# Optimization experiments

Hardware: AMD Instinct MI355X
Metric: run time of the kernel (lower is better)

Reference implementation:

```python
import jax, jax.numpy as jnp
import numpy as np

N = 100000          # nodes
E = 1_600_000       # edges (avg degree 16)
IN, H, OUT = 64, 128, 64


def _gcn(x, src, tgt, w, W, b, n):
    """PyG GCNConv with add_self_loops=True and edge weights.
    Zero-weight edges contribute nothing to degree or aggregation, so the
    torch code's boolean edge masking is reproduced exactly by zeroed weights.
    """
    h = x @ W.T                                           # [n, out]
    deg = jax.ops.segment_sum(w, tgt, num_segments=n) + 1.0  # +1 self-loop weight
    dinv = jnp.where(deg > 0, jax.lax.rsqrt(deg), 0.0)    # [n]
    norm = dinv[src] * w * dinv[tgt]                      # [e]
    agg = jax.ops.segment_sum(h[src] * norm[:, None], tgt, num_segments=n)
    # self-loop message: h_i * dinv_i * 1 * dinv_i
    return agg + h * (dinv * dinv)[:, None] + b


def setup_inputs() -> dict:
    key = jax.random.key(0)
    ks = jax.random.split(key, 12)
    def lin(k, o, i):
        return jax.random.normal(k, (o, i), dtype=jnp.float32) / np.sqrt(i)
    return {
        "x": jax.random.normal(ks[0], (N, IN), dtype=jnp.float32),
        "edge_index": jax.random.randint(ks[1], (2, E), 0, N),
        "edge_weight": jax.random.normal(ks[2], (E,), dtype=jnp.float32),
        "W1p": lin(ks[3], H, IN),  "b1p": jnp.zeros((H,), jnp.float32),
        "W1n": lin(ks[4], H, IN),  "b1n": jnp.zeros((H,), jnp.float32),
        "W2p": lin(ks[5], OUT, H), "b2p": jnp.zeros((OUT,), jnp.float32),
        "W2n": lin(ks[6], OUT, H), "b2n": jnp.zeros((OUT,), jnp.float32),
    }


def reference(x, edge_index, edge_weight, W1p, b1p, W1n, b1n, W2p, b2p, W2n, b2n):
    src, tgt = edge_index[0], edge_index[1]
    n = x.shape[0]
    wp = jnp.where(edge_weight >= 0, edge_weight, 0.0)    # pos subgraph
    wn = jnp.where(edge_weight < 0, -edge_weight, 0.0)    # |neg| subgraph
    h = jax.nn.relu(_gcn(x, src, tgt, wp, W1p, b1p, n)
                    - _gcn(x, src, tgt, wn, W1n, b1n, n))
    out = jax.nn.relu(_gcn(h, src, tgt, wp, W2p, b2p, n)
                      - _gcn(h, src, tgt, wn, W2n, b2n, n))
    return out
```

## Files before the change

kernel.cpp:

```cpp
#include <hip/hip_runtime.h>
#include <hip/hip_fp16.h>
#include <cstddef>

#define TPB 256
#define BSH 9
#define BTGT 512
#define EPA 16
#define ACHUNK (EPA * TPB)
#define LSTR 160
#define CAP 10240

typedef _Float16 f16x8 __attribute__((ext_vector_type(8)));
typedef float    f32x4 __attribute__((ext_vector_type(4)));

__global__ __launch_bounds__(256) void bucket_scatter_kernel(
        const int* __restrict__ tgt, const int* __restrict__ src,
        const float* __restrict__ ew, int* __restrict__ cnt_pad,
        int2* __restrict__ recs, int E) {
    __shared__ int lcnt[256];
    __shared__ int lbase[256];
    const int tid = threadIdx.x;
    lcnt[tid] = 0;
    __syncthreads();
    const int base = blockIdx.x * ACHUNK + tid;
    int px[EPA], pw[EPA], mr[EPA], mb[EPA];
#pragma unroll
    for (int j = 0; j < EPA; ++j) {
        int e = base + j * TPB;
        if (e < E) {
            int t = tgt[e], s = src[e];
            float w = ew[e];
            int flag = (w < 0.0f) ? 1 : 0;
            mb[j] = t >> BSH;
            px[j] = ((t & (BTGT - 1)) << 23) | (s << 6) | flag;
            pw[j] = __float_as_int(w);
            mr[j] = atomicAdd(&lcnt[mb[j]], 1);
        }
    }
    __syncthreads();
    if (lcnt[tid]) lbase[tid] = atomicAdd(&cnt_pad[tid * 16], lcnt[tid]);
    __syncthreads();
#pragma unroll
    for (int j = 0; j < EPA; ++j) {
        int e = base + j * TPB;
        if (e < E) {
            int sl = lbase[mb[j]] + mr[j];
            if (sl < CAP)
                recs[(size_t)mb[j] * CAP + sl] = make_int2(px[j], pw[j]);
        }
    }
}

__global__ __launch_bounds__(512) void csr_build_kernel(
        const int* __restrict__ cnt_pad, const int2* __restrict__ recs,
        int2* __restrict__ rowse, int2* __restrict__ edat,
        float* __restrict__ dinvp, float* __restrict__ dinvn,
        const float* __restrict__ x,
        const float* __restrict__ W1p, const float* __restrict__ W1n,
        const float* __restrict__ W2p, const float* __restrict__ W2n,
        __half* __restrict__ xs, __half* __restrict__ w16, int n) {
    __shared__ int   hcnt[BTGT];
    __shared__ int   cur[BTGT];
    __shared__ int   sm[BTGT];
    __shared__ float sdp[BTGT];
    __shared__ float sdn[BTGT];
    const int b = blockIdx.x, tid = threadIdx.x;
    int cnt = cnt_pad[b * 16]; if (cnt > CAP) cnt = CAP;
    const int beg = b * CAP, end = beg + cnt;
    hcnt[tid] = 0;
    sdp[tid] = 0.f;
    sdn[tid] = 0.f;
    __syncthreads();
    for (int i = beg + tid; i < end; i += 512) {
        int2 r = recs[i];
        int tl = ((unsigned)r.x) >> 23;
        atomicAdd(&hcnt[tl], 1);
        float w = __int_as_float(r.y);
        if (w > 0.0f)      atomicAdd(&sdp[tl], w);
        else if (w < 0.0f) atomicAdd(&sdn[tl], -w);
    }
    __syncthreads();
    int own = hcnt[tid];
    sm[tid] = own;
    __syncthreads();
#pragma unroll
    for (int off = 1; off < 512; off <<= 1) {
        int add = (tid >= off) ? sm[tid - off] : 0;
        __syncthreads();
        sm[tid] += add;
        __syncthreads();
    }
    int excl = sm[tid] - own;
    cur[tid] = beg + excl;
    const int t0 = b << BSH;
    const int t = t0 + tid;
    if (t < n) {
        rowse[t] = make_int2(beg + excl, beg + excl + own);
        float dp = rsqrtf(sdp[tid] + 1.0f);
        float dn = rsqrtf(sdn[tid] + 1.0f);
        dinvp[t] = dp; dinvn[t] = dn;
        sdp[tid] = dp; sdn[tid] = dn;
    }
    __syncthreads();
    for (int i = beg + tid; i < end; i += 512) {
        int2 r = recs[i];
        int tl = ((unsigned)r.x) >> 23;
        int slot = atomicAdd(&cur[tl], 1);
        float w = __int_as_float(r.y);
        int flag = r.x & 1;
        float nv = w * (flag ? sdn[tl] : sdp[tl]);
        int srcflag = (((r.x >> 6) & 0x1FFFF) << 8) | (flag << 7) | flag;
        edat[slot] = make_int2(srcflag, __float_as_int(nv));
    }
    for (int it = tid; it < (BTGT << 5); it += 512) {
        int j = it >> 5, jp = it & 31;
        int tt = t0 + j;
        if (tt >= n) continue;
        float2 v = *(const float2*)(x + (size_t)tt * 64 + jp * 2);
        float dp = sdp[j], dn = sdn[j];
        __half2* xr = (__half2*)(xs + (size_t)tt * 128);
        xr[jp]      = __floats2half2_rn(v.x * dp, v.y * dp);
        xr[jp + 32] = __floats2half2_rn(v.x * dn, v.y * dn);
    }
    if (b == 0) {
        for (int q = tid; q < 16384; q += 512) {
            const float* Wsrc = (q < 4096) ? W1p : (q < 8192) ? W1n
                              : (q < 12288) ? W2p : W2n;
            float2 v = *(const float2*)(Wsrc + (size_t)(q & 4095) * 2);
            ((__half2*)w16)[q] = __floats2half2_rn(v.x, v.y);
        }
    }
}

__global__ __launch_bounds__(256) void gatherX_kernel(
        const int2* __restrict__ rowse, const int2* __restrict__ edat,
        const __half* __restrict__ xs,
        const float* __restrict__ dinvp, const float* __restrict__ dinvn,
        __half* __restrict__ agg, int n) {
    const int lane = threadIdx.x & 63;
    int t = (blockIdx.x * blockDim.x + threadIdx.x) >> 6;
    if (t >= n) return;
    t = __builtin_amdgcn_readfirstlane(t);
    const char* xB = (const char*)xs;
    int2 se = rowse[t];
    int beg = se.x, end = se.y;
    float aP[8], aN[8];
#pragma unroll
    for (int j = 0; j < 8; ++j) { aP[j] = 0.f; aN[j] = 0.f; }
    int e = beg;
    for (; e + 7 < end; e += 8) {
        unsigned long long dv[8];
#pragma unroll
        for (int j = 0; j < 8; ++j)
            dv[j] = __builtin_nontemporal_load(
                        (const unsigned long long*)(edat + e + j));
        const __half* r[8];
        float nvv[8];
        int fl[8];
#pragma unroll
        for (int j = 0; j < 8; ++j) {
            unsigned dx = (unsigned)dv[j];
            r[j]   = (const __half*)(xB + (dx & 0xFFFFFF80u));
            nvv[j] = __int_as_float((int)(dv[j] >> 32));
            fl[j]  = dx & 1;
        }
#pragma unroll
        for (int j = 0; j < 8; ++j) {
            float c = __half2float(r[j][lane]) * nvv[j];
            if (fl[j]) aN[j] += c; else aP[j] += c;
        }
    }
    for (; e + 3 < end; e += 4) {
        unsigned long long dv[4];
#pragma unroll
        for (int j = 0; j < 4; ++j)
            dv[j] = __builtin_nontemporal_load(
                        (const unsigned long long*)(edat + e + j));
#pragma unroll
        for (int j = 0; j < 4; ++j) {
            unsigned dx = (unsigned)dv[j];
            const __half* r = (const __half*)(xB + (dx & 0xFFFFFF80u));
            float c = __half2float(r[lane]) * __int_as_float((int)(dv[j] >> 32));
            if (dx & 1) aN[j] += c; else aP[j] += c;
        }
    }
    for (; e < end; ++e) {
        unsigned long long dv = __builtin_nontemporal_load(
                                    (const unsigned long long*)(edat + e));
        unsigned dx = (unsigned)dv;
        const __half* r = (const __half*)(xB + (dx & 0xFFFFFF80u));
        float c = __half2float(r[lane]) * __int_as_float((int)(dv >> 32));
        if (dx & 1) aN[0] += c; else aP[0] += c;
    }
    float accP = ((aP[0] + aP[1]) + (aP[2] + aP[3]))
               + ((aP[4] + aP[5]) + (aP[6] + aP[7]));
    float accN = ((aN[0] + aN[1]) + (aN[2] + aN[3]))
               + ((aN[4] + aN[5]) + (aN[6] + aN[7]));
    float sp = dinvp[t], sn = dinvn[t];
    accP += sp * __half2float(xs[(size_t)t * 128 + lane]);
    accN -= sn * __half2float(xs[(size_t)t * 128 + 64 + lane]);
    __builtin_nontemporal_store(__half_as_ushort((__half)accP),
        (unsigned short*)(agg + (size_t)t * 128 + lane));
    __builtin_nontemporal_store(__half_as_ushort((__half)accN),
        (unsigned short*)(agg + (size_t)t * 128 + 64 + lane));
}

__global__ __launch_bounds__(256) void gemm12_mfma(
        const __half* agg,
        const __half* __restrict__ w1p, const __half* __restrict__ w1n,
        const float* __restrict__ b1p, const float* __restrict__ b1n,
        const __half* __restrict__ w2p, const __half* __restrict__ w2n,
        const float* __restrict__ dinvp, const float* __restrict__ dinvn,
        __half* g2, int n) {
    __shared__ _Float16 tile[4][16 * LSTR];
    const int lane = threadIdx.x & 63;
    const int wv = threadIdx.x >> 6;
    _Float16* T = tile[wv];
    const int m = lane & 15, quad = lane >> 4;
    const int row0 = (blockIdx.x * 4 + wv) * 16;
    if (row0 >= n) return;
    int arow = row0 + m; if (arow > n - 1) arow = n - 1;

    f32x4 acc[8];
#pragma unroll
    for (int t = 0; t < 8; ++t) acc[t] = (f32x4){0.f, 0.f, 0.f, 0.f};
#pragma unroll
    for (int kc = 0; kc < 4; ++kc) {
        f16x8 a = *(const f16x8*)(agg + (size_t)arow * 128 + kc * 32 + quad * 8);
        const __half* W = (kc < 2) ? w1p : w1n;
        const int ko = (kc & 1) * 32 + quad * 8;
#pragma unroll
        for (int t = 0; t < 8; ++t) {
            f16x8 bfr = *(const f16x8*)(W + (size_t)(t * 16 + m) * 64 + ko);
            acc[t] = __builtin_amdgcn_mfma_f32_16x16x32_f16(a, bfr, acc[t], 0, 0, 0);
        }
    }
#pragma unroll
    for (int t = 0; t < 8; ++t) {
        int col = t * 16 + m;
        float bd = b1p[col] - b1n[col];
#pragma unroll
        for (int r = 0; r < 4; ++r)
            T[(quad * 4 + r) * LSTR + col] = (_Float16)fmaxf(acc[t][r] + bd, 0.f);
    }

    f32x4 acc2[8];
#pragma unroll
    for (int t = 0; t < 8; ++t) acc2[t] = (f32x4){0.f, 0.f, 0.f, 0.f};
#pragma unroll
    for (int kc = 0; kc < 4; ++kc) {
        f16x8 a = *(const f16x8*)(T + m * LSTR + kc * 32 + quad * 8);
#pragma unroll
        for (int t = 0; t < 8; ++t) {
            const __half* W = (t < 4) ? w2p : w2n;
            f16x8 bfr = *(const f16x8*)(W + (size_t)((t & 3) * 16 + m) * 128 + kc * 32 + quad * 8);
            acc2[t] = __builtin_amdgcn_mfma_f32_16x16x32_f16(a, bfr, acc2[t], 0, 0, 0);
        }
    }
    float sp[4], sn[4]; int rows[4];
#pragma unroll
    for (int r = 0; r < 4; ++r) {
        int rw = row0 + quad * 4 + r;
        rows[r] = rw;
        sp[r] = (rw < n) ? dinvp[rw] : 0.f;
        sn[r] = (rw < n) ? dinvn[rw] : 0.f;
    }
#pragma unroll
    for (int t = 0; t < 8; ++t) {
        int col = (t < 4 ? 0 : 64) + (t & 3) * 16 + m;
#pragma unroll
        for (int r = 0; r < 4; ++r)
            if (rows[r] < n) {
                float s = (t < 4) ? sp[r] : sn[r];
                g2[(size_t)rows[r] * 128 + col] = (__half)(acc2[t][r] * s);
            }
    }
}

__global__ __launch_bounds__(256) void gather64_kernel(
        const int2* __restrict__ rowse, const int2* __restrict__ edat,
        const __half* __restrict__ g2,
        const float* __restrict__ dinvp, const float* __restrict__ dinvn,
        const float* __restrict__ bp, const float* __restrict__ bn,
        float* __restrict__ out, int n) {
    const int lane = threadIdx.x & 63;
    int t = (blockIdx.x * blockDim.x + threadIdx.x) >> 6;
    if (t >= n) return;
    t = __builtin_amdgcn_readfirstlane(t);
    const char* gB = (const char*)g2;
    int2 se = rowse[t];
    int beg = se.x, end = se.y;
    float ac[8];
#pragma unroll
    for (int j = 0; j < 8; ++j) ac[j] = 0.f;
    int e = beg;
    for (; e + 7 < end; e += 8) {
        unsigned long long dv[8];
#pragma unroll
        for (int j = 0; j < 8; ++j)
            dv[j] = __builtin_nontemporal_load(
                        (const unsigned long long*)(edat + e + j));
#pragma unroll
        for (int j = 0; j < 8; ++j) {
            unsigned dx = (unsigned)dv[j];
            const __half* r = (const __half*)(gB + (dx & 0xFFFFFF80u));
            ac[j] += __half2float(r[lane]) * __int_as_float((int)(dv[j] >> 32));
        }
    }
    for (; e + 3 < end; e += 4) {
        unsigned long long dv[4];
#pragma unroll
        for (int j = 0; j < 4; ++j)
            dv[j] = __builtin_nontemporal_load(
                        (const unsigned long long*)(edat + e + j));
#pragma unroll
        for (int j = 0; j < 4; ++j) {
            unsigned dx = (unsigned)dv[j];
            const __half* r = (const __half*)(gB + (dx & 0xFFFFFF80u));
            ac[j] += __half2float(r[lane]) * __int_as_float((int)(dv[j] >> 32));
        }
    }
    for (; e < end; ++e) {
        unsigned long long dv = __builtin_nontemporal_load(
                                    (const unsigned long long*)(edat + e));
        unsigned dx = (unsigned)dv;
        const __half* r = (const __half*)(gB + (dx & 0xFFFFFF80u));
        ac[0] += __half2float(r[lane]) * __int_as_float((int)(dv >> 32));
    }
    float acc = ((ac[0] + ac[1]) + (ac[2] + ac[3]))
              + ((ac[4] + ac[5]) + (ac[6] + ac[7]));
    const float dp = dinvp[t], dn = dinvn[t];
    float hpv = __half2float(g2[(size_t)t * 128 + lane]);
    float hnv = __half2float(g2[(size_t)t * 128 + 64 + lane]);
    float o = acc + hpv * dp + bp[lane] - hnv * dn - bn[lane];
    __builtin_nontemporal_store(fmaxf(o, 0.f), out + (size_t)t * 64 + lane);
}

extern "C" void kernel_launch(void* const* d_in, const int* in_sizes, int n_in,
                              void* d_out, int out_size, void* d_ws, size_t ws_size,
                              hipStream_t stream) {
    const float* x   = (const float*)d_in[0];
    const int*   ei  = (const int*)d_in[1];
    const float* ew  = (const float*)d_in[2];
    const float* W1p = (const float*)d_in[3];
    const float* b1p = (const float*)d_in[4];
    const float* W1n = (const float*)d_in[5];
    const float* b1n = (const float*)d_in[6];
    const float* W2p = (const float*)d_in[7];
    const float* b2p = (const float*)d_in[8];
    const float* W2n = (const float*)d_in[9];
    const float* b2n = (const float*)d_in[10];

    const int E = in_sizes[2];
    const int n = in_sizes[0] / 64;
    const int nb = (n + BTGT - 1) >> BSH;
    const int* src = ei;
    const int* tgt = ei + E;

    int* wsi     = (int*)d_ws;
    int* cnt_pad = wsi;
    size_t o = 4096;
    int2*  rowse  = (int2*)(wsi + o);   o += 2 * (size_t)n;
    float* dinvp  = (float*)(wsi + o);  o += n;
    float* dinvn  = (float*)(wsi + o);  o += n;
    o = (o + 3) & ~(size_t)3;
    __half* xs  = (__half*)(wsi + o);   o += (size_t)n * 64;
    __half* w16 = (__half*)(wsi + o);   o += 16384;
    __half* w1p16 = w16, *w1n16 = w16 + 8192, *w2p16 = w16 + 16384, *w2n16 = w16 + 24576;
    int2* recs = (int2*)(wsi + o);      o += 2 * (size_t)nb * CAP;
    int2* edat = (int2*)(wsi + o);      o += 2 * (size_t)nb * CAP;
    __half* agg = (__half*)(wsi + o);   o += (size_t)n * 64;
    __half* g2  = agg;
    float*  out = (float*)d_out;

    hipMemsetAsync(cnt_pad, 0, 4096 * sizeof(int), stream);

    const int gridA = (E + ACHUNK - 1) / ACHUNK;
    const int gridW = (n * 64 + TPB - 1) / TPB;
    const int gridF = (n + 63) / 64;

    bucket_scatter_kernel<<<gridA, TPB, 0, stream>>>(tgt, src, ew, cnt_pad, recs, E);
    csr_build_kernel<<<nb, 512, 0, stream>>>(cnt_pad, recs, rowse, edat,
                                             dinvp, dinvn, x,
                                             W1p, W1n, W2p, W2n, xs, w16, n);
    gatherX_kernel<<<gridW, TPB, 0, stream>>>(rowse, edat, xs, dinvp, dinvn, agg, n);
    gemm12_mfma<<<gridF, TPB, 0, stream>>>(agg, w1p16, w1n16, b1p, b1n,
                                           w2p16, w2n16, dinvp, dinvn, g2, n);
    gather64_kernel<<<gridW, TPB, 0, stream>>>(rowse, edat, g2, dinvp, dinvn,
                                               b2p, b2n, out, n);
}
```

Before: 328.0 us.

## Make fused GEMM kernel persistent with register-resident weights and next-tile prefetch

Rewrites the two-layer MFMA GEMM so that each block handles one 16-row tile at a time, with its four waves splitting the output columns. Each wave loads its weight fragments into registers once, and the block loops over tiles with a grid-stride loop capped at a fixed grid size. The next tile's input rows are prefetched while the current tile is stored to shared memory, and the shared tile is shrunk and shared by the block. This is meant to cut repeated weight loads and overlap input loads with compute. In exchange it adds two block-wide barriers per tile and lowers parallelism per tile.

New measurement: 298.2 us. -9.1%, faster.

```diff
diff --git a/kernel.cpp b/kernel.cpp
--- a/kernel.cpp
+++ b/kernel.cpp
@@ -7,8 +7,9 @@
 #define BTGT 512
 #define EPA 16
 #define ACHUNK (EPA * TPB)
-#define LSTR 160
+#define LSTR 136
 #define CAP 10240
+#define GGRID 1024
 
 typedef _Float16 f16x8 __attribute__((ext_vector_type(8)));
 typedef float    f32x4 __attribute__((ext_vector_type(4)));
@@ -205,75 +206,95 @@
         (unsigned short*)(agg + (size_t)t * 128 + 64 + lane));
 }
 
-__global__ __launch_bounds__(256) void gemm12_mfma(
+__global__ __launch_bounds__(256, 2) void gemm12_mfma(
         const __half* agg,
         const __half* __restrict__ w1p, const __half* __restrict__ w1n,
         const float* __restrict__ b1p, const float* __restrict__ b1n,
         const __half* __restrict__ w2p, const __half* __restrict__ w2n,
         const float* __restrict__ dinvp, const float* __restrict__ dinvn,
         __half* g2, int n) {
-    __shared__ _Float16 tile[4][16 * LSTR];
+    __shared__ _Float16 T[16 * LSTR];
     const int lane = threadIdx.x & 63;
     const int wv = threadIdx.x >> 6;
-    _Float16* T = tile[wv];
     const int m = lane & 15, quad = lane >> 4;
-    const int row0 = (blockIdx.x * 4 + wv) * 16;
-    if (row0 >= n) return;
-    int arow = row0 + m; if (arow > n - 1) arow = n - 1;
-
-    f32x4 acc[8];
-#pragma unroll
-    for (int t = 0; t < 8; ++t) acc[t] = (f32x4){0.f, 0.f, 0.f, 0.f};
+    const int t0 = 2 * wv, t1 = t0 + 1;
+    const int ntile = (n + 15) >> 4;
+
+    f16x8 B1a[4], B1b[4], B2a[4], B2b[4];
+    const __half* W2 = (t0 < 4) ? w2p : w2n;
 #pragma unroll
     for (int kc = 0; kc < 4; ++kc) {
-        f16x8 a = *(const f16x8*)(agg + (size_t)arow * 128 + kc * 32 + quad * 8);
-        const __half* W = (kc < 2) ? w1p : w1n;
+        const __half* W1 = (kc < 2) ? w1p : w1n;
         const int ko = (kc & 1) * 32 + quad * 8;
-#pragma unroll
-        for (int t = 0; t < 8; ++t) {
-            f16x8 bfr = *(const f16x8*)(W + (size_t)(t * 16 + m) * 64 + ko);
-            acc[t] = __builtin_amdgcn_mfma_f32_16x16x32_f16(a, bfr, acc[t], 0, 0, 0);
-        }
-    }
-#pragma unroll
-    for (int t = 0; t < 8; ++t) {
-        int col = t * 16 + m;
-        float bd = b1p[col] - b1n[col];
-#pragma unroll
-        for (int r = 0; r < 4; ++r)
-            T[(quad * 4 + r) * LSTR + col] = (_Float16)fmaxf(acc[t][r] + bd, 0.f);
-    }
-
-    f32x4 acc2[8];
-#pragma unroll
-    for (int t = 0; t < 8; ++t) acc2[t] = (f32x4){0.f, 0.f, 0.f, 0.f};
-#pragma unroll
-    for (int kc = 0; kc < 4; ++kc) {
-        f16x8 a = *(const f16x8*)(T + m * LSTR + kc * 32 + quad * 8);
-#pragma unroll
-        for (int t = 0; t < 8; ++t) {
-            const __half* W = (t < 4) ? w2p : w2n;
-            f16x8 bfr = *(const f16x8*)(W + (size_t)((t & 3) * 16 + m) * 128 + kc * 32 + quad * 8);
-            acc2[t] = __builtin_amdgcn_mfma_f32_16x16x32_f16(a, bfr, acc2[t], 0, 0, 0);
-        }
-    }
-    float sp[4], sn[4]; int rows[4];
-#pragma unroll
-    for (int r = 0; r < 4; ++r) {
-        int rw = row0 + quad * 4 + r;
-        rows[r] = rw;
-        sp[r] = (rw < n) ? dinvp[rw] : 0.f;
-        sn[r] = (rw < n) ? dinvn[rw] : 0.f;
-    }
-#pragma unroll
-    for (int t = 0; t < 8; ++t) {
-        int col = (t < 4 ? 0 : 64) + (t & 3) * 16 + m;
+        B1a[kc] = *(const f16x8*)(W1 + (size_t)(t0 * 16 + m) * 64 + ko);
+        B1b[kc] = *(const f16x8*)(W1 + (size_t)(t1 * 16 + m) * 64 + ko);
+        B2a[kc] = *(const f16x8*)(W2 + (size_t)((t0 & 3) * 16 + m) * 128 + kc * 32 + quad * 8);
+        B2b[kc] = *(const f16x8*)(W2 + (size_t)((t1 & 3) * 16 + m) * 128 + kc * 32 + quad * 8);
+    }
+    const float bd0 = b1p[t0 * 16 + m] - b1n[t0 * 16 + m];
+    const float bd1 = b1p[t1 * 16 + m] - b1n[t1 * 16 + m];
+
+    int tile = blockIdx.x;
+    f16x8 a1c[4];
+    if (tile < ntile) {
+        int arow = tile * 16 + m; if (arow > n - 1) arow = n - 1;
+#pragma unroll
+        for (int kc = 0; kc < 4; ++kc)
+            a1c[kc] = *(const f16x8*)(agg + (size_t)arow * 128 + kc * 32 + quad * 8);
+    }
+
+    for (; tile < ntile; tile += gridDim.x) {
+        const int row0 = tile * 16;
+        f32x4 acc0 = (f32x4){0.f, 0.f, 0.f, 0.f};
+        f32x4 acc1 = (f32x4){0.f, 0.f, 0.f, 0.f};
+#pragma unroll
+        for (int kc = 0; kc < 4; ++kc) {
+            acc0 = __builtin_amdgcn_mfma_f32_16x16x32_f16(a1c[kc], B1a[kc], acc0, 0, 0, 0);
+            acc1 = __builtin_amdgcn_mfma_f32_16x16x32_f16(a1c[kc], B1b[kc], acc1, 0, 0, 0);
+        }
+        float sp[4], sn[4]; int rows[4];
+#pragma unroll
+        for (int r = 0; r < 4; ++r) {
+            int rw = row0 + quad * 4 + r;
+            rows[r] = rw;
+            sp[r] = (rw < n) ? dinvp[rw] : 0.f;
+            sn[r] = (rw < n) ? dinvn[rw] : 0.f;
+        }
+#pragma unroll
+        for (int r = 0; r < 4; ++r) {
+            T[(quad * 4 + r) * LSTR + t0 * 16 + m] = (_Float16)fmaxf(acc0[r] + bd0, 0.f);
+            T[(quad * 4 + r) * LSTR + t1 * 16 + m] = (_Float16)fmaxf(acc1[r] + bd1, 0.f);
+        }
+        const int ntile_i = tile + gridDim.x;
+        f16x8 a1nx[4];
+        if (ntile_i < ntile) {
+            int arow = ntile_i * 16 + m; if (arow > n - 1) arow = n - 1;
+#pragma unroll
+            for (int kc = 0; kc < 4; ++kc)
+                a1nx[kc] = *(const f16x8*)(agg + (size_t)arow * 128 + kc * 32 + quad * 8);
+        }
+        __syncthreads();
+        f16x8 a2[4];
+#pragma unroll
+        for (int kc = 0; kc < 4; ++kc)
+            a2[kc] = *(const f16x8*)(T + m * LSTR + kc * 32 + quad * 8);
+        __syncthreads();
+        f32x4 c0 = (f32x4){0.f, 0.f, 0.f, 0.f};
+        f32x4 c1 = (f32x4){0.f, 0.f, 0.f, 0.f};
+#pragma unroll
+        for (int kc = 0; kc < 4; ++kc) {
+            c0 = __builtin_amdgcn_mfma_f32_16x16x32_f16(a2[kc], B2a[kc], c0, 0, 0, 0);
+            c1 = __builtin_amdgcn_mfma_f32_16x16x32_f16(a2[kc], B2b[kc], c1, 0, 0, 0);
+        }
+        const float* dsel0 = (t0 < 4) ? sp : sn;
 #pragma unroll
         for (int r = 0; r < 4; ++r)
             if (rows[r] < n) {
-                float s = (t < 4) ? sp[r] : sn[r];
-                g2[(size_t)rows[r] * 128 + col] = (__half)(acc2[t][r] * s);
+                g2[(size_t)rows[r] * 128 + t0 * 16 + m] = (__half)(c0[r] * dsel0[r]);
+                g2[(size_t)rows[r] * 128 + t1 * 16 + m] = (__half)(c1[r] * dsel0[r]);
             }
+#pragma unroll
+        for (int kc = 0; kc < 4; ++kc) a1c[kc] = a1nx[kc];
     }
 }
 
@@ -377,7 +398,8 @@
 
     const int gridA = (E + ACHUNK - 1) / ACHUNK;
     const int gridW = (n * 64 + TPB - 1) / TPB;
-    const int gridF = (n + 63) / 64;
+    const int ntile = (n + 15) / 16;
+    const int gridF = (ntile < GGRID) ? ntile : GGRID;
 
     bucket_scatter_kernel<<<gridA, TPB, 0, stream>>>(tgt, src, ew, cnt_pad, recs, E);
     csr_build_kernel<<<nb, 512, 0, stream>>>(cnt_pad, recs, rowse, edat,
```
